# Performance work log

Hardware: AMD Instinct MI355X
Metric: run time of the kernel (lower is better)

## Reference

```python
import jax, jax.numpy as jnp
import numpy as np

N, K, R = 32768, 4096, 256

def setup_inputs() -> dict:
    key = jax.random.key(0)
    k1, k2, k3 = jax.random.split(key, 3)
    H = jax.random.normal(k1, (N, R), dtype=jnp.float32)
    L = jax.random.normal(k2, (K, R), dtype=jnp.float32)
    W_I = jax.random.normal(k3, (R, R), dtype=jnp.float32)
    return {"H": H, "L": L, "W_I": W_I}

def reference(H, L, W_I):
    # Q = W_I @ L^T : (r, k)
    Q = jnp.einsum('rs,ks->rk', W_I, L)
    # M_I = H @ Q : (n, k)
    M_I = jnp.einsum('nr,rk->nk', H, Q)
    A_I = jax.nn.softmax(M_I, axis=1)
    # C_I = A_I @ L : (n, r)
    C_I = jnp.einsum('nk,kr->nr', A_I, L)
    return (C_I, A_I)
```

## Files before the change

kernel.cpp:

```cpp
#include <hip/hip_runtime.h>
#include <hip/hip_bf16.h>
#include <math.h>
#include <stdint.h>

constexpr int N_ROWS = 32768;
constexpr int K_DIM  = 4096;
constexpr int R_DIM  = 256;
constexpr int KP     = 3 * R_DIM;
constexpr int KB     = K_DIM / 128;

typedef __bf16 bf16x8 __attribute__((ext_vector_type(8)));
typedef float  f32x4  __attribute__((ext_vector_type(4)));
typedef unsigned short u16x8 __attribute__((ext_vector_type(8)));
typedef unsigned short u16x4 __attribute__((ext_vector_type(4)));

__device__ __forceinline__ unsigned short f2bf(float x) {
    unsigned u = __float_as_uint(x);
    u += 0x7fffu + ((u >> 16) & 1u);
    return (unsigned short)(u >> 16);
}
__device__ __forceinline__ float bf2f(unsigned short h) {
    return __uint_as_float((unsigned)h << 16);
}

__device__ __forceinline__ void gl2lds16(const void* gptr, void* lptr) {
    __builtin_amdgcn_global_load_lds(
        (const __attribute__((address_space(1))) unsigned int*)gptr,
        (__attribute__((address_space(3))) unsigned int*)lptr,
        16, 0, 0);
}

__global__ __launch_bounds__(256)
void gemm_mfma_nt(const unsigned short* __restrict__ A,
                  const unsigned short* __restrict__ B,
                  float* __restrict__ Mout,
                  float* __restrict__ Pm, float* __restrict__ Ps,
                  int M, int N, int Kc)
{
    __shared__ __align__(16) unsigned short As[128 * 32];
    __shared__ __align__(16) unsigned short Bs[128 * 32];
    __shared__ float pm_s[128][2], ps_s[128][2];
    __shared__ float pmc[128];

    const int tid  = threadIdx.x;
    const int wave = tid >> 6, lane = tid & 63;
    const int wm = wave >> 1, wn = wave & 1;

    const int bid = blockIdx.x;
    const int xg = bid >> 10;
    const int yb = (bid >> 5) & 31;
    const int xi = bid & 31;
    const long m0 = (long)(xg * 32 + xi) * 128;
    const long n0 = (long)yb * 128;

    f32x4 acc[4][4] = {};

    const int srow  = lane >> 2;
    const int skoff = (lane & 3) * 8;
    const int c0 = wave, c1 = wave + 4;
    const int kq = (lane >> 4) * 8;
    const int mr = lane & 15;

    for (int k0 = 0; k0 < Kc; k0 += 32) {
        gl2lds16(A + (m0 + c0 * 16 + srow) * (long)Kc + k0 + skoff, &As[c0 * 512]);
        gl2lds16(A + (m0 + c1 * 16 + srow) * (long)Kc + k0 + skoff, &As[c1 * 512]);
        gl2lds16(B + (n0 + c0 * 16 + srow) * (long)Kc + k0 + skoff, &Bs[c0 * 512]);
        gl2lds16(B + (n0 + c1 * 16 + srow) * (long)Kc + k0 + skoff, &Bs[c1 * 512]);
        __syncthreads();

        bf16x8 af[4], bfr[4];
#pragma unroll
        for (int t = 0; t < 4; ++t) {
            af[t]  = *(const bf16x8*)&As[(wm * 64 + t * 16 + mr) * 32 + kq];
            bfr[t] = *(const bf16x8*)&Bs[(wn * 64 + t * 16 + mr) * 32 + kq];
        }
#pragma unroll
        for (int i = 0; i < 4; ++i)
#pragma unroll
            for (int j = 0; j < 4; ++j)
                acc[i][j] = __builtin_amdgcn_mfma_f32_16x16x32_bf16(
                    af[i], bfr[j], acc[i][j], 0, 0, 0);
        __syncthreads();
    }

    const int col = lane & 15, rquad = (lane >> 4) * 4;

#pragma unroll
    for (int i = 0; i < 4; ++i) {
#pragma unroll
        for (int r = 0; r < 4; ++r) {
            float mx = fmaxf(fmaxf(acc[i][0][r], acc[i][1][r]),
                             fmaxf(acc[i][2][r], acc[i][3][r]));
#pragma unroll
            for (int off = 1; off < 16; off <<= 1)
                mx = fmaxf(mx, __shfl_xor(mx, off));
            float sm = 0.f;
#pragma unroll
            for (int j = 0; j < 4; ++j) sm += __expf(acc[i][j][r] - mx);
#pragma unroll
            for (int off = 1; off < 16; off <<= 1)
                sm += __shfl_xor(sm, off);
            if (mr == 0) {
                const int rw = wm * 64 + i * 16 + rquad + r;
                pm_s[rw][wn] = mx;
                ps_s[rw][wn] = sm;
            }
        }
    }
    __syncthreads();
    if (tid < 128) {
        const float ma = pm_s[tid][0], mb = pm_s[tid][1];
        const float mx = fmaxf(ma, mb);
        const float s  = ps_s[tid][0] * __expf(ma - mx) +
                         ps_s[tid][1] * __expf(mb - mx);
        pmc[tid] = mx;
        Pm[(m0 + tid) * KB + yb] = mx;
        Ps[(m0 + tid) * KB + yb] = s;
    }
    __syncthreads();

    unsigned short* E = (unsigned short*)Mout;
#pragma unroll
    for (int i = 0; i < 4; ++i) {
#pragma unroll
        for (int r = 0; r < 4; ++r) {
            const int rw = wm * 64 + i * 16 + rquad + r;
            const float mx = pmc[rw];
            unsigned short* ep =
                E + (m0 + rw) * 8192L + 4096 + n0 + wn * 64 + col;
#pragma unroll
            for (int j = 0; j < 4; ++j)
                ep[j * 16] = f2bf(__expf(acc[i][j][r] - mx));
        }
    }
}

__global__ __launch_bounds__(256)
void finalize_ms(const float* __restrict__ Pm, const float* __restrict__ Ps,
                 float* __restrict__ SMm, float* __restrict__ SMi)
{
    const long row = (long)blockIdx.x * 256 + threadIdx.x;
    const float4* pm = (const float4*)(Pm + row * KB);
    const float4* ps = (const float4*)(Ps + row * KB);
    float4 v[8];
    float mx = -3.4e38f;
#pragma unroll
    for (int q = 0; q < 8; ++q) {
        v[q] = pm[q];
        mx = fmaxf(mx, fmaxf(fmaxf(v[q].x, v[q].y), fmaxf(v[q].z, v[q].w)));
    }
    float s = 0.f;
#pragma unroll
    for (int q = 0; q < 8; ++q) {
        float4 w = ps[q];
        s += w.x * __expf(v[q].x - mx) + w.y * __expf(v[q].y - mx) +
             w.z * __expf(v[q].z - mx) + w.w * __expf(v[q].w - mx);
    }
    SMm[row] = mx;
    SMi[row] = 1.f / s;
}

__global__ __launch_bounds__(512)
void softmax_av_pv(float* Aout,
                   const unsigned short* __restrict__ LT,
                   const float* __restrict__ Pm,
                   const float* __restrict__ SMm,
                   const float* __restrict__ SMi,
                   float* __restrict__ C)
{
    __shared__ __align__(16) unsigned short Bs[R_DIM * 64];
    __shared__ __align__(16) unsigned short As[64 * 64];
    __shared__ float cs[64][32];

    const int tid  = threadIdx.x;
    const int wave = tid >> 6, lane = tid & 63;
    const long m0 = (long)blockIdx.x * 64;

    {
        const int i0 = tid * 4;
        const int r  = i0 >> 5;
        const int b  = i0 & 31;
        const float m = SMm[m0 + r], inv = SMi[m0 + r];
        const float4 pv = *(const float4*)(Pm + (m0 + r) * KB + b);
        cs[r][b + 0] = __expf(pv.x - m) * inv;
        cs[r][b + 1] = __expf(pv.y - m) * inv;
        cs[r][b + 2] = __expf(pv.z - m) * inv;
        cs[r][b + 3] = __expf(pv.w - m) * inv;
    }
    __syncthreads();

    f32x4 acc[2][4] = {};
    const int wm = wave >> 2, wn = wave & 3;
    const int mr = lane & 15;
    const int kq16 = (lane >> 4) * 16;

    const int arow0 = wave * 4 + (lane >> 4);
    const int arow1 = 32 + arow0;
    const int acolE = (lane & 15) * 4;
    const unsigned short* const ep0 =
        (const unsigned short*)Aout + (m0 + arow0) * 8192L + 4096 + acolE;
    const unsigned short* const ep1 =
        (const unsigned short*)Aout + (m0 + arow1) * 8192L + 4096 + acolE;
    float* const gp0 = Aout + (m0 + arow0) * (long)K_DIM + acolE;
    float* const gp1 = Aout + (m0 + arow1) * (long)K_DIM + acolE;
    const int ab0 = (arow0 * 128 + acolE * 2) ^ ((arow0 & 7) << 4);
    const int ab1 = (arow1 * 128 + acolE * 2) ^ ((arow1 & 7) << 4);

    u16x4 va0 = *(const u16x4*)ep0;
    u16x4 va1 = *(const u16x4*)ep1;

    constexpr int NT = K_DIM / 64;
    for (int t = 0; t < NT; ++t) {
        const int k0 = t * 64;
        if (t == NT - 1) __syncthreads();

#pragma unroll
        for (int q = 0; q < 4; ++q) {
            const int rbase = q * 64 + wave * 8;
            const int rloc  = rbase + (lane >> 3);
            const int phys  = (lane & 7) * 16;
            const int kbyte = phys ^ ((rloc & 7) << 4);
            gl2lds16((const char*)LT + (long)rloc * (K_DIM * 2) + (long)k0 * 2 + kbyte,
                     &Bs[rbase * 64]);
        }
        {
            const float c0 = cs[arow0][t >> 1], c1 = cs[arow1][t >> 1];
            float a0 = bf2f(va0[0]) * c0, a1 = bf2f(va0[1]) * c0;
            float a2 = bf2f(va0[2]) * c0, a3 = bf2f(va0[3]) * c0;
            *(float4*)(gp0 + k0) = make_float4(a0, a1, a2, a3);
            u16x4 u0;
            u0[0] = f2bf(a0); u0[1] = f2bf(a1); u0[2] = f2bf(a2); u0[3] = f2bf(a3);
            *(u16x4*)((char*)As + ab0) = u0;

            float b0 = bf2f(va1[0]) * c1, b1 = bf2f(va1[1]) * c1;
            float b2 = bf2f(va1[2]) * c1, b3 = bf2f(va1[3]) * c1;
            *(float4*)(gp1 + k0) = make_float4(b0, b1, b2, b3);
            u16x4 u1;
            u1[0] = f2bf(b0); u1[1] = f2bf(b1); u1[2] = f2bf(b2); u1[3] = f2bf(b3);
            *(u16x4*)((char*)As + ab1) = u1;
        }
        __syncthreads();

        if (t + 1 < NT) {
            va0 = *(const u16x4*)(ep0 + (t + 1) * 64);
            va1 = *(const u16x4*)(ep1 + (t + 1) * 64);
        }

#pragma unroll
        for (int ks = 0; ks < 2; ++ks) {
            bf16x8 af[2], bfr[4];
#pragma unroll
            for (int tt = 0; tt < 2; ++tt) {
                const int arow = wm * 32 + tt * 16 + mr;
                const int ab = (arow * 128 + ks * 64 + kq16) ^ ((arow & 7) << 4);
                af[tt] = *(const bf16x8*)((const char*)As + ab);
            }
#pragma unroll
            for (int tt = 0; tt < 4; ++tt) {
                const int brow = wn * 64 + tt * 16 + mr;
                const int bb = (brow * 128 + ks * 64 + kq16) ^ ((brow & 7) << 4);
                bfr[tt] = *(const bf16x8*)((const char*)Bs + bb);
            }
#pragma unroll
            for (int i = 0; i < 2; ++i)
#pragma unroll
                for (int j = 0; j < 4; ++j)
                    acc[i][j] = __builtin_amdgcn_mfma_f32_16x16x32_bf16(
                        af[i], bfr[j], acc[i][j], 0, 0, 0);
        }
        __syncthreads();
    }

    const int col = lane & 15, rquad = (lane >> 4) * 4;
#pragma unroll
    for (int i = 0; i < 2; ++i) {
        const int lrow0 = wm * 32 + i * 16 + rquad;
#pragma unroll
        for (int j = 0; j < 4; ++j) {
            float* p = C + (m0 + lrow0) * (long)R_DIM + wn * 64 + j * 16 + col;
#pragma unroll
            for (int r = 0; r < 4; ++r)
                p[(long)r * R_DIM] = acc[i][j][r];
        }
    }
}

__global__ __launch_bounds__(256)
void prep_B(const float* __restrict__ L, unsigned short* __restrict__ Bp)
{
    const long i = (long)blockIdx.x * 256 + threadIdx.x;
    const long k = i >> 8; const int r = (int)(i & 255);
    const float x = L[i];
    const unsigned short hi = f2bf(x);
    const unsigned short lo = f2bf(x - bf2f(hi));
    unsigned short* row = Bp + k * KP;
    row[r] = hi; row[R_DIM + r] = lo; row[2 * R_DIM + r] = hi;
}

__global__ __launch_bounds__(256)
void prep_LT(const float* __restrict__ L, unsigned short* __restrict__ LT)
{
    const long i = (long)blockIdx.x * 256 + threadIdx.x;
    const long r = i >> 12; const long k = i & 4095;
    LT[r * K_DIM + k] = f2bf(L[k * R_DIM + r]);
}

template<bool BT>
__global__ __launch_bounds__(256)
void gemm128(const float* __restrict__ A, const float* __restrict__ B,
             float* __restrict__ C, int M, int N, int Kc)
{
    __shared__ __align__(16) float Asl[16][132];
    __shared__ __align__(16) float Bsl[16][132];

    const int tid = threadIdx.x;
    const int tx = tid & 15, ty = tid >> 4;
    const long m0 = (long)blockIdx.x * 128;
    const long n0 = (long)blockIdx.y * 128;

    float acc[8][8];
#pragma unroll
    for (int i = 0; i < 8; ++i)
#pragma unroll
        for (int j = 0; j < 8; ++j) acc[i][j] = 0.f;

    for (int k0 = 0; k0 < Kc; k0 += 16) {
#pragma unroll
        for (int q = 0; q < 2; ++q) {
            int fi = tid + 256 * q, row = fi >> 2, col = (fi & 3) * 4;
            float4 v = *(const float4*)(A + (m0 + row) * (long)Kc + k0 + col);
            Asl[col + 0][row] = v.x; Asl[col + 1][row] = v.y;
            Asl[col + 2][row] = v.z; Asl[col + 3][row] = v.w;
        }
        if (BT) {
#pragma unroll
            for (int q = 0; q < 2; ++q) {
                int fi = tid + 256 * q, row = fi >> 2, col = (fi & 3) * 4;
                float4 v = *(const float4*)(B + (n0 + row) * (long)Kc + k0 + col);
                Bsl[col + 0][row] = v.x; Bsl[col + 1][row] = v.y;
                Bsl[col + 2][row] = v.z; Bsl[col + 3][row] = v.w;
            }
        } else {
#pragma unroll
            for (int q = 0; q < 2; ++q) {
                int fi = tid + 256 * q, row = fi >> 5, col = (fi & 31) * 4;
                float4 v = *(const float4*)(B + (k0 + row) * (long)N + n0 + col);
                *(float4*)&Bsl[row][col] = v;
            }
        }
        __syncthreads();
#pragma unroll
        for (int kk = 0; kk < 16; ++kk) {
            float a[8], b[8];
            *(float4*)&a[0] = *(const float4*)&Asl[kk][ty * 8];
            *(float4*)&a[4] = *(const float4*)&Asl[kk][ty * 8 + 4];
            *(float4*)&b[0] = *(const float4*)&Bsl[kk][tx * 8];
            *(float4*)&b[4] = *(const float4*)&Bsl[kk][tx * 8 + 4];
#pragma unroll
            for (int i = 0; i < 8; ++i)
#pragma unroll
                for (int j = 0; j < 8; ++j)
                    acc[i][j] = fmaf(a[i], b[j], acc[i][j]);
        }
        __syncthreads();
    }
#pragma unroll
    for (int i = 0; i < 8; ++i) {
        float* p = C + (m0 + ty * 8 + i) * (long)N + n0 + tx * 8;
        *(float4*)p       = make_float4(acc[i][0], acc[i][1], acc[i][2], acc[i][3]);
        *(float4*)(p + 4) = make_float4(acc[i][4], acc[i][5], acc[i][6], acc[i][7]);
    }
}

__global__ __launch_bounds__(256)
void gemm128_hl(const float* __restrict__ A, const float* __restrict__ B,
                unsigned short* __restrict__ Ap, int M, int N, int Kc)
{
    __shared__ __align__(16) float Asl[16][132];
    __shared__ __align__(16) float Bsl[16][132];

    const int tid = threadIdx.x;
    const int tx = tid & 15, ty = tid >> 4;
    const long m0 = (long)blockIdx.x * 128;
    const long n0 = (long)blockIdx.y * 128;

    float acc[8][8];
#pragma unroll
    for (int i = 0; i < 8; ++i)
#pragma unroll
        for (int j = 0; j < 8; ++j) acc[i][j] = 0.f;

    for (int k0 = 0; k0 < Kc; k0 += 16) {
#pragma unroll
        for (int q = 0; q < 2; ++q) {
            int fi = tid + 256 * q, row = fi >> 2, col = (fi & 3) * 4;
            float4 v = *(const float4*)(A + (m0 + row) * (long)Kc + k0 + col);
            Asl[col + 0][row] = v.x; Asl[col + 1][row] = v.y;
            Asl[col + 2][row] = v.z; Asl[col + 3][row] = v.w;
        }
#pragma unroll
        for (int q = 0; q < 2; ++q) {
            int fi = tid + 256 * q, row = fi >> 5, col = (fi & 31) * 4;
            float4 v = *(const float4*)(B + (k0 + row) * (long)N + n0 + col);
            *(float4*)&Bsl[row][col] = v;
        }
        __syncthreads();
#pragma unroll
        for (int kk = 0; kk < 16; ++kk) {
            float a[8], b[8];
            *(float4*)&a[0] = *(const float4*)&Asl[kk][ty * 8];
            *(float4*)&a[4] = *(const float4*)&Asl[kk][ty * 8 + 4];
            *(float4*)&b[0] = *(const float4*)&Bsl[kk][tx * 8];
            *(float4*)&b[4] = *(const float4*)&Bsl[kk][tx * 8 + 4];
#pragma unroll
            for (int i = 0; i < 8; ++i)
#pragma unroll
                for (int j = 0; j < 8; ++j)
                    acc[i][j] = fmaf(a[i], b[j], acc[i][j]);
        }
        __syncthreads();
    }
#pragma unroll
    for (int i = 0; i < 8; ++i) {
        const long row = m0 + ty * 8 + i;
        const int  cb  = (int)n0 + tx * 8;
        u16x8 vh, vl;
#pragma unroll
        for (int j = 0; j < 8; ++j) {
            const float x = acc[i][j];
            const unsigned short hi = f2bf(x);
            vh[j] = hi;
            vl[j] = f2bf(x - bf2f(hi));
        }
        unsigned short* rp = Ap + row * KP;
        *(u16x8*)(rp + cb)             = vh;
        *(u16x8*)(rp + R_DIM + cb)     = vh;
        *(u16x8*)(rp + 2 * R_DIM + cb) = vl;
    }
}

__global__ __launch_bounds__(256)
void softmax_rows(float* __restrict__ Mio)
{
    const long n  = blockIdx.x;
    float* row    = Mio + n * (long)K_DIM;
    const int tid = threadIdx.x;

    float4 v[4];
    float lmax = -3.4e38f;
#pragma unroll
    for (int q = 0; q < 4; ++q) {
        v[q] = ((const float4*)row)[tid + 256 * q];
        lmax = fmaxf(lmax, fmaxf(fmaxf(v[q].x, v[q].y), fmaxf(v[q].z, v[q].w)));
    }
    __shared__ float redmax[4], redsum[4];
#pragma unroll
    for (int off = 32; off > 0; off >>= 1)
        lmax = fmaxf(lmax, __shfl_xor(lmax, off));
    if ((tid & 63) == 0) redmax[tid >> 6] = lmax;
    __syncthreads();
    const float gmax = fmaxf(fmaxf(redmax[0], redmax[1]), fmaxf(redmax[2], redmax[3]));

    float lsum = 0.f;
#pragma unroll
    for (int q = 0; q < 4; ++q) {
        v[q].x = __expf(v[q].x - gmax); v[q].y = __expf(v[q].y - gmax);
        v[q].z = __expf(v[q].z - gmax); v[q].w = __expf(v[q].w - gmax);
        lsum += v[q].x + v[q].y + v[q].z + v[q].w;
    }
#pragma unroll
    for (int off = 32; off > 0; off >>= 1)
        lsum += __shfl_xor(lsum, off);
    if ((tid & 63) == 0) redsum[tid >> 6] = lsum;
    __syncthreads();
    const float inv = 1.f / (redsum[0] + redsum[1] + redsum[2] + redsum[3]);
#pragma unroll
    for (int q = 0; q < 4; ++q) {
        v[q].x *= inv; v[q].y *= inv; v[q].z *= inv; v[q].w *= inv;
        ((float4*)row)[tid + 256 * q] = v[q];
    }
}

extern "C" void kernel_launch(void* const* d_in, const int* in_sizes, int n_in,
                              void* d_out, int out_size, void* d_ws, size_t ws_size,
                              hipStream_t stream)
{
    const float* H  = (const float*)d_in[0];
    const float* L  = (const float*)d_in[1];
    const float* Wi = (const float*)d_in[2];

    float* Cout = (float*)d_out;
    float* Aout = (float*)d_out + (size_t)N_ROWS * R_DIM;

    const size_t szAp = (size_t)N_ROWS * KP * 2;
    const size_t szBp = (size_t)K_DIM * KP * 2;
    const size_t szLT = (size_t)R_DIM * K_DIM * 2;
    const size_t szPm = (size_t)N_ROWS * KB * 4;
    const size_t szPs = (size_t)N_ROWS * KB * 4;
    const size_t szSM = (size_t)N_ROWS * 4;

    if (ws_size >= szAp + szBp + szLT + szPm + szPs + 2 * szSM) {
        char* w = (char*)d_ws;
        unsigned short* Ap = (unsigned short*)w;                 w += szAp;
        unsigned short* Bp = (unsigned short*)w;                 w += szBp;
        unsigned short* LT = (unsigned short*)w;                 w += szLT;
        float* Pm  = (float*)w;                                  w += szPm;
        float* Ps  = (float*)w;                                  w += szPs;
        float* SMm = (float*)w;                                  w += szSM;
        float* SMi = (float*)w;

        gemm128_hl<<<dim3(N_ROWS / 128, R_DIM / 128), 256, 0, stream>>>(
            H, Wi, Ap, N_ROWS, R_DIM, R_DIM);
        prep_B<<<dim3((K_DIM * R_DIM) / 256), 256, 0, stream>>>(L, Bp);
        prep_LT<<<dim3((R_DIM * K_DIM) / 256), 256, 0, stream>>>(L, LT);
        gemm_mfma_nt<<<dim3((N_ROWS / 128) * (K_DIM / 128)), 256, 0, stream>>>(
            Ap, Bp, Aout, Pm, Ps, N_ROWS, K_DIM, KP);
        finalize_ms<<<dim3(N_ROWS / 256), 256, 0, stream>>>(Pm, Ps, SMm, SMi);
        softmax_av_pv<<<dim3(N_ROWS / 64), 512, 0, stream>>>(
            Aout, LT, Pm, SMm, SMi, Cout);
    } else {
        gemm128<false><<<dim3(N_ROWS / 128, R_DIM / 128), 256, 0, stream>>>(
            H, Wi, Cout, N_ROWS, R_DIM, R_DIM);
        gemm128<true><<<dim3(N_ROWS / 128, K_DIM / 128), 256, 0, stream>>>(
            Cout, L, Aout, N_ROWS, K_DIM, R_DIM);
        softmax_rows<<<dim3(N_ROWS), 256, 0, stream>>>(Aout);
        gemm128<false><<<dim3(N_ROWS / 128, R_DIM / 128), 256, 0, stream>>>(
            Aout, L, Cout, N_ROWS, R_DIM, K_DIM);
    }
}
```

Baseline: 1.150 ms.

## Double-buffer LDS tiles in softmax_av_pv and precompute per-block scale factors

```diff
diff --git a/kernel.cpp b/kernel.cpp
--- a/kernel.cpp
+++ b/kernel.cpp
@@ -136,60 +136,53 @@
 }
 
 __global__ __launch_bounds__(256)
-void finalize_ms(const float* __restrict__ Pm, const float* __restrict__ Ps,
+void finalize_ms(const float* __restrict__ Pm, float* __restrict__ Ps,
                  float* __restrict__ SMm, float* __restrict__ SMi)
 {
     const long row = (long)blockIdx.x * 256 + threadIdx.x;
     const float4* pm = (const float4*)(Pm + row * KB);
-    const float4* ps = (const float4*)(Ps + row * KB);
-    float4 v[8];
+    float4* ps = (float4*)(Ps + row * KB);
+    float4 v[8], w[8];
     float mx = -3.4e38f;
 #pragma unroll
     for (int q = 0; q < 8; ++q) {
         v[q] = pm[q];
+        w[q] = ps[q];
         mx = fmaxf(mx, fmaxf(fmaxf(v[q].x, v[q].y), fmaxf(v[q].z, v[q].w)));
     }
     float s = 0.f;
 #pragma unroll
     for (int q = 0; q < 8; ++q) {
-        float4 w = ps[q];
-        s += w.x * __expf(v[q].x - mx) + w.y * __expf(v[q].y - mx) +
-             w.z * __expf(v[q].z - mx) + w.w * __expf(v[q].w - mx);
-    }
+        s += w[q].x * __expf(v[q].x - mx) + w[q].y * __expf(v[q].y - mx) +
+             w[q].z * __expf(v[q].z - mx) + w[q].w * __expf(v[q].w - mx);
+    }
+    const float inv = 1.f / s;
     SMm[row] = mx;
-    SMi[row] = 1.f / s;
-}
-
-__global__ __launch_bounds__(512)
+    SMi[row] = inv;
+#pragma unroll
+    for (int q = 0; q < 8; ++q) {
+        float4 c;
+        c.x = __expf(v[q].x - mx) * inv;
+        c.y = __expf(v[q].y - mx) * inv;
+        c.z = __expf(v[q].z - mx) * inv;
+        c.w = __expf(v[q].w - mx) * inv;
+        ps[q] = c;
+    }
+}
+
+__global__ __launch_bounds__(512, 4)
 void softmax_av_pv(float* Aout,
                    const unsigned short* __restrict__ LT,
-                   const float* __restrict__ Pm,
-                   const float* __restrict__ SMm,
-                   const float* __restrict__ SMi,
+                   const float* __restrict__ CS,
                    float* __restrict__ C)
 {
-    __shared__ __align__(16) unsigned short Bs[R_DIM * 64];
-    __shared__ __align__(16) unsigned short As[64 * 64];
-    __shared__ float cs[64][32];
+    __shared__ __align__(16) unsigned short Bs[2][R_DIM * 64];
+    __shared__ __align__(16) unsigned short As[2][64 * 64];
 
     const int tid  = threadIdx.x;
     const int wave = tid >> 6, lane = tid & 63;
     const long m0 = (long)blockIdx.x * 64;
 
-    {
-        const int i0 = tid * 4;
-        const int r  = i0 >> 5;
-        const int b  = i0 & 31;
-        const float m = SMm[m0 + r], inv = SMi[m0 + r];
-        const float4 pv = *(const float4*)(Pm + (m0 + r) * KB + b);
-        cs[r][b + 0] = __expf(pv.x - m) * inv;
-        cs[r][b + 1] = __expf(pv.y - m) * inv;
-        cs[r][b + 2] = __expf(pv.z - m) * inv;
-        cs[r][b + 3] = __expf(pv.w - m) * inv;
-    }
-    __syncthreads();
-
-    f32x4 acc[2][4] = {};
     const int wm = wave >> 2, wn = wave & 3;
     const int mr = lane & 15;
     const int kq16 = (lane >> 4) * 16;
@@ -205,15 +198,13 @@
     float* const gp1 = Aout + (m0 + arow1) * (long)K_DIM + acolE;
     const int ab0 = (arow0 * 128 + acolE * 2) ^ ((arow0 & 7) << 4);
     const int ab1 = (arow1 * 128 + acolE * 2) ^ ((arow1 & 7) << 4);
-
-    u16x4 va0 = *(const u16x4*)ep0;
-    u16x4 va1 = *(const u16x4*)ep1;
-
+    const float* const cs0 = CS + (m0 + arow0) * KB;
+    const float* const cs1 = CS + (m0 + arow1) * KB;
+
+    f32x4 acc[2][4] = {};
     constexpr int NT = K_DIM / 64;
-    for (int t = 0; t < NT; ++t) {
-        const int k0 = t * 64;
-        if (t == NT - 1) __syncthreads();
-
+
+    auto stage_B = [&](int buf, int k0) {
 #pragma unroll
         for (int q = 0; q < 4; ++q) {
             const int rbase = q * 64 + wave * 8;
@@ -221,29 +212,47 @@
             const int phys  = (lane & 7) * 16;
             const int kbyte = phys ^ ((rloc & 7) << 4);
             gl2lds16((const char*)LT + (long)rloc * (K_DIM * 2) + (long)k0 * 2 + kbyte,
-                     &Bs[rbase * 64]);
-        }
-        {
-            const float c0 = cs[arow0][t >> 1], c1 = cs[arow1][t >> 1];
-            float a0 = bf2f(va0[0]) * c0, a1 = bf2f(va0[1]) * c0;
-            float a2 = bf2f(va0[2]) * c0, a3 = bf2f(va0[3]) * c0;
-            *(float4*)(gp0 + k0) = make_float4(a0, a1, a2, a3);
-            u16x4 u0;
-            u0[0] = f2bf(a0); u0[1] = f2bf(a1); u0[2] = f2bf(a2); u0[3] = f2bf(a3);
-            *(u16x4*)((char*)As + ab0) = u0;
-
-            float b0 = bf2f(va1[0]) * c1, b1 = bf2f(va1[1]) * c1;
-            float b2 = bf2f(va1[2]) * c1, b3 = bf2f(va1[3]) * c1;
-            *(float4*)(gp1 + k0) = make_float4(b0, b1, b2, b3);
-            u16x4 u1;
-            u1[0] = f2bf(b0); u1[1] = f2bf(b1); u1[2] = f2bf(b2); u1[3] = f2bf(b3);
-            *(u16x4*)((char*)As + ab1) = u1;
-        }
-        __syncthreads();
-
+                     &Bs[buf][rbase * 64]);
+        }
+    };
+    auto emit_A = [&](int buf, int t1, u16x4 va0, u16x4 va1) {
+        const int b  = t1 >> 1;
+        const int k0 = t1 * 64;
+        const float c0 = cs0[b], c1 = cs1[b];
+        float a0 = bf2f(va0[0]) * c0, a1 = bf2f(va0[1]) * c0;
+        float a2 = bf2f(va0[2]) * c0, a3 = bf2f(va0[3]) * c0;
+        *(float4*)(gp0 + k0) = make_float4(a0, a1, a2, a3);
+        u16x4 u0;
+        u0[0] = f2bf(a0); u0[1] = f2bf(a1); u0[2] = f2bf(a2); u0[3] = f2bf(a3);
+        *(u16x4*)((char*)As[buf] + ab0) = u0;
+
+        float b0 = bf2f(va1[0]) * c1, b1 = bf2f(va1[1]) * c1;
+        float b2 = bf2f(va1[2]) * c1, b3 = bf2f(va1[3]) * c1;
+        *(float4*)(gp1 + k0) = make_float4(b0, b1, b2, b3);
+        u16x4 u1;
+        u1[0] = f2bf(b0); u1[1] = f2bf(b1); u1[2] = f2bf(b2); u1[3] = f2bf(b3);
+        *(u16x4*)((char*)As[buf] + ab1) = u1;
+    };
+
+    stage_B(0, 0);
+    {
+        u16x4 e0a = *(const u16x4*)ep0;
+        u16x4 e0b = *(const u16x4*)ep1;
+        emit_A(0, 0, e0a, e0b);
+    }
+    u16x4 va0 = *(const u16x4*)(ep0 + 64);
+    u16x4 va1 = *(const u16x4*)(ep1 + 64);
+    __syncthreads();
+
+    for (int t = 0; t < NT; ++t) {
+        const int cur = t & 1, nxt = cur ^ 1;
         if (t + 1 < NT) {
-            va0 = *(const u16x4*)(ep0 + (t + 1) * 64);
-            va1 = *(const u16x4*)(ep1 + (t + 1) * 64);
+            stage_B(nxt, (t + 1) * 64);
+            emit_A(nxt, t + 1, va0, va1);
+        }
+        if (t + 2 < NT) {
+            va0 = *(const u16x4*)(ep0 + (t + 2) * 64);
+            va1 = *(const u16x4*)(ep1 + (t + 2) * 64);
         }
 
 #pragma unroll
@@ -251,15 +260,15 @@
             bf16x8 af[2], bfr[4];
 #pragma unroll
             for (int tt = 0; tt < 2; ++tt) {
-                const int arow = wm * 32 + tt * 16 + mr;
-                const int ab = (arow * 128 + ks * 64 + kq16) ^ ((arow & 7) << 4);
-                af[tt] = *(const bf16x8*)((const char*)As + ab);
+                const int ar = wm * 32 + tt * 16 + mr;
+                const int ab = (ar * 128 + ks * 64 + kq16) ^ ((ar & 7) << 4);
+                af[tt] = *(const bf16x8*)((const char*)As[cur] + ab);
             }
 #pragma unroll
             for (int tt = 0; tt < 4; ++tt) {
-                const int brow = wn * 64 + tt * 16 + mr;
-                const int bb = (brow * 128 + ks * 64 + kq16) ^ ((brow & 7) << 4);
-                bfr[tt] = *(const bf16x8*)((const char*)Bs + bb);
+                const int br = wn * 64 + tt * 16 + mr;
+                const int bb = (br * 128 + ks * 64 + kq16) ^ ((br & 7) << 4);
+                bfr[tt] = *(const bf16x8*)((const char*)Bs[cur] + bb);
             }
 #pragma unroll
             for (int i = 0; i < 2; ++i)
@@ -517,7 +526,7 @@
             Ap, Bp, Aout, Pm, Ps, N_ROWS, K_DIM, KP);
         finalize_ms<<<dim3(N_ROWS / 256), 256, 0, stream>>>(Pm, Ps, SMm, SMi);
         softmax_av_pv<<<dim3(N_ROWS / 64), 512, 0, stream>>>(
-            Aout, LT, Pm, SMm, SMi, Cout);
+            Aout, LT, Ps, Cout);
     } else {
         gemm128<false><<<dim3(N_ROWS / 128, R_DIM / 128), 256, 0, stream>>>(
             H, Wi, Cout, N_ROWS, R_DIM, R_DIM);
```

Measured after the change: 1.148 ms. No clear change (-0.2%).
